# Kernel optimization log

Hardware: AMD Instinct MI355X
Metric: run time of the kernel (lower is better)

The kernel has to match this reference:

```python
import jax, jax.numpy as jnp
import numpy as np

BN_EPS = 1e-3


def _three_nn(unknown, known):
    # unknown: [B, N2, 3] query points; known: [B, N1, 3]
    # returns squared distances and indices of the 3 nearest known points
    # (CUDA three_nn returns squared euclidean distances).
    d2 = (jnp.sum(unknown * unknown, -1)[:, :, None]
          + jnp.sum(known * known, -1)[:, None, :]
          - 2.0 * jnp.einsum('bnd,bmd->bnm', unknown, known))  # [B, N2, N1]
    neg_top, ind = jax.lax.top_k(-d2, 3)                        # [B, N2, 3]
    dist2 = jnp.maximum(-neg_top, 0.0)
    return dist2, ind


def _conv_bn_relu(x, W, b, gamma, beta, mean, var):
    # x: [B, C_in, N]; W: [C_out, C_in] (1x1 conv); inference-mode BN
    y = jnp.einsum('oc,bcn->bon', W, x) + b[None, :, None]
    scale = gamma / jnp.sqrt(var + BN_EPS)
    y = (y - mean[None, :, None]) * scale[None, :, None] + beta[None, :, None]
    return jax.nn.relu(y)


def setup_inputs() -> dict:
    key = jax.random.key(0)
    ks = jax.random.split(key, 12)
    B, N1, N2, C1, C2, H = 2, 4096, 16384, 256, 128, 256
    return {
        'points1': jax.random.normal(ks[0], (B, 3, N1), jnp.float32),
        'points2': jax.random.normal(ks[1], (B, 3, N2), jnp.float32),
        'features1': jax.random.normal(ks[2], (B, C1, N1), jnp.float32),
        'features2': jax.random.normal(ks[3], (B, C2, N2), jnp.float32),
        'W1': jax.random.normal(ks[4], (H, C1 + C2), jnp.float32) * 0.05,
        'b1': jax.random.normal(ks[5], (H,), jnp.float32) * 0.05,
        'gamma1': jnp.ones((H,), jnp.float32),
        'beta1': jnp.zeros((H,), jnp.float32),
        'mean1': jax.random.normal(ks[6], (H,), jnp.float32) * 0.1,
        'var1': jax.random.uniform(ks[7], (H,), jnp.float32, 0.5, 1.5),
        'W2': jax.random.normal(ks[8], (H, H), jnp.float32) * 0.05,
        'b2': jax.random.normal(ks[9], (H,), jnp.float32) * 0.05,
        'gamma2': jnp.ones((H,), jnp.float32),
        'beta2': jnp.zeros((H,), jnp.float32),
        'mean2': jax.random.normal(ks[10], (H,), jnp.float32) * 0.1,
        'var2': jax.random.uniform(ks[11], (H,), jnp.float32, 0.5, 1.5),
    }


def reference(points1, points2, features1, features2,
              W1, b1, gamma1, beta1, mean1, var1,
              W2, b2, gamma2, beta2, mean2, var2):
    # 3-NN of each dense point (points2) among coarse points (points1)
    unknown = jnp.swapaxes(points2, 1, 2)  # [B, N2, 3]
    known = jnp.swapaxes(points1, 1, 2)    # [B, N1, 3]
    dist, ind = _three_nn(unknown, known)  # dist: squared distances [B, N2, 3]
    dist = dist * dist                     # forward squares again (as in source)
    dist = jnp.maximum(dist, 1e-10)
    inv = 1.0 / dist
    weights = inv / jnp.sum(inv, axis=2, keepdims=True)  # [B, N2, 3]

    # gather features of the 3 neighbors: features1 [B, C1, N1] -> [B, N2, 3, C1]
    f1 = jnp.swapaxes(features1, 1, 2)  # [B, N1, C1]
    gathered = jax.vmap(lambda f, i: f[i])(f1, ind)  # [B, N2, 3, C1]
    interp = jnp.einsum('bnkc,bnk->bcn', gathered, weights)  # [B, C1, N2]

    x = jnp.concatenate([interp, features2], axis=1)  # [B, C1+C2, N2]
    x = _conv_bn_relu(x, W1, b1, gamma1, beta1, mean1, var1)
    x = _conv_bn_relu(x, W2, b2, gamma2, beta2, mean2, var2)
    return x
```

## Files before the change

### kernel.cpp

```cpp
#include <hip/hip_runtime.h>
#include <cstdint>
#include <cstddef>

#define N1 4096
#define N2 16384
#define C1 256
#define C2 128
#define HH 256
#define K1 384
#define BQ 32768
#define KPAD 392
#define NCH 8

typedef float  f32x4  __attribute__((ext_vector_type(4)));
typedef __bf16 bf16x8 __attribute__((ext_vector_type(8)));
typedef __bf16 bf16x4 __attribute__((ext_vector_type(4)));

__device__ __forceinline__ float exact_dd(float ux, float uy, float uz,
                                          float su, float4 p) {
  float dot = __fadd_rn(__fadd_rn(__fmul_rn(ux, p.x), __fmul_rn(uy, p.y)),
                        __fmul_rn(uz, p.z));
  return __builtin_fmaf(dot, -2.0f, __fadd_rn(su, p.w));
}

__device__ __forceinline__ float4 load_pt(const float* __restrict__ p1b,
                                          int j) {
  float x = p1b[j], y = p1b[N1 + j], z = p1b[2 * N1 + j];
  float sk = __fadd_rn(__fadd_rn(__fmul_rn(x, x), __fmul_rn(y, y)),
                       __fmul_rn(z, z));
  return make_float4(x, y, z, sk);
}

#define LEXINS(da, db, dc, ia, ib, ic, dd, jj)                                 \
  {                                                                            \
    bool ca = ((dd) < (da)) || ((dd) == (da) && (jj) < (ia));                  \
    bool cb = ((dd) < (db)) || ((dd) == (db) && (jj) < (ib));                  \
    bool cc = ((dd) < (dc)) || ((dd) == (dc) && (jj) < (ic));                  \
    dc = cb ? (db) : (cc ? (dd) : (dc));                                       \
    ic = cb ? (ib) : (cc ? (jj) : (ic));                                       \
    db = ca ? (da) : (cb ? (dd) : (db));                                       \
    ib = ca ? (ia) : (cb ? (jj) : (ib));                                       \
    da = ca ? (dd) : (da);                                                     \
    ia = ca ? (jj) : (ia);                                                     \
  }

#define KMIN4(K1_, K2_, K3_, K4_, x)                                           \
  {                                                                            \
    float n1 = fminf((K1_), (x));                                              \
    float n2 = __builtin_amdgcn_fmed3f((K1_), (x), (K2_));                     \
    float n3 = __builtin_amdgcn_fmed3f((K2_), (x), (K3_));                     \
    float n4 = __builtin_amdgcn_fmed3f((K3_), (x), (K4_));                     \
    K1_ = n1; K2_ = n2; K3_ = n3; K4_ = n4;                                    \
  }

#define POINTQ(ux, uy, uz, su, px, py, pz, pw, jj, Ka, Kb, Kc, Kd)             \
  {                                                                            \
    float dot_ = __fadd_rn(                                                    \
        __fadd_rn(__fmul_rn((ux), (px)), __fmul_rn((uy), (py))),               \
        __fmul_rn((uz), (pz)));                                                \
    float dd_ = __builtin_fmaf(dot_, -2.0f, __fadd_rn((su), (pw)));            \
    float xk_ = __uint_as_float((__float_as_uint(dd_) & 0xFFFFF000u) |         \
                                ((unsigned)(jj) & 0x00000FFFu));               \
    KMIN4(Ka, Kb, Kc, Kd, xk_);                                                \
  }

__global__ __launch_bounds__(256) void k_front(
    const float* __restrict__ p1, const float* __restrict__ p2,
    const float* __restrict__ f1,
    const float* __restrict__ W1, const float* __restrict__ W2,
    const float* __restrict__ b1, const float* __restrict__ g1,
    const float* __restrict__ be1, const float* __restrict__ mm1,
    const float* __restrict__ vv1,
    const float* __restrict__ b2, const float* __restrict__ g2,
    const float* __restrict__ be2, const float* __restrict__ mm2,
    const float* __restrict__ vv2,
    __bf16* __restrict__ W1b, __bf16* __restrict__ W2b,
    float* __restrict__ scsh, float* __restrict__ f1T,
    float* __restrict__ keybuf) {
#pragma clang fp contract(off)
  __shared__ __align__(16) float smemf[64 * 65];
  const int bx = blockIdx.x;
  const int t = threadIdx.x;

  if (bx < 384) {
    int idx = bx * 256 + t;
    if (idx < HH * K1) W1b[idx] = (__bf16)W1[idx];
    if (idx < HH * HH) W2b[idx] = (__bf16)W2[idx];
    if (idx < HH) {
      float sc = g1[idx] / sqrtf(vv1[idx] + 1e-3f);
      scsh[idx]          = sc;
      scsh[HH + idx]     = fmaf(b1[idx] - mm1[idx], sc, be1[idx]);
      float s2 = g2[idx] / sqrtf(vv2[idx] + 1e-3f);
      scsh[2 * HH + idx] = s2;
      scsh[3 * HH + idx] = fmaf(b2[idx] - mm2[idx], s2, be2[idx]);
    }
    return;
  }

  if (bx < 896) {
    float (*tile)[65] = (float(*)[65])smemf;
    const int bz = bx - 384;
    const int b = bz >> 8;
    const int rest = bz & 255;
    const int ct = rest >> 6;
    const int ntb = (rest & 63) << 6;
    const int ln = t & 63, g = t >> 6;

    const float* src = f1 + ((size_t)b * C1 + ct * 64) * N1 + ntb;
    for (int k = 0; k < 16; ++k) {
      int c = (k << 2) + g;
      tile[c][ln] = src[(size_t)c * N1 + ln];
    }
    __syncthreads();
    float* dst = f1T + ((size_t)b * N1 + ntb) * C1 + ct * 64;
    for (int k = 0; k < 16; ++k) {
      int nn = (k << 2) + g;
      dst[(size_t)nn * C1 + ln] = tile[ln][nn];
    }
    return;
  }

  float4* spts = (float4*)smemf;
  const int bz = bx - 896;
  const int ch = bz & (NCH - 1);
  const int qt = bz >> 3;
  const int b  = qt >> 5;
  const int nA = ((qt & 31) << 9) + t;
  const int nB = nA + 256;

  const float* p1b = p1 + (size_t)b * 3 * N1;
  {
    int j = ch * 512 + t;
    spts[t]       = load_pt(p1b, j);
    spts[t + 256] = load_pt(p1b, j + 256);
  }

  const float* p2b = p2 + (size_t)b * 3 * N2;
  float uxA = p2b[nA], uyA = p2b[N2 + nA], uzA = p2b[2 * N2 + nA];
  float suA = __fadd_rn(__fadd_rn(__fmul_rn(uxA, uxA), __fmul_rn(uyA, uyA)),
                        __fmul_rn(uzA, uzA));
  float uxB = p2b[nB], uyB = p2b[N2 + nB], uzB = p2b[2 * N2 + nB];
  float suB = __fadd_rn(__fadd_rn(__fmul_rn(uxB, uxB), __fmul_rn(uyB, uyB)),
                        __fmul_rn(uzB, uzB));
  __syncthreads();

  const int j0 = ch * 512;
  float KaA = 3.0e38f, KbA = 3.0e38f, KcA = 3.0e38f, KdA = 3.0e38f;
  float KaB = 3.0e38f, KbB = 3.0e38f, KcB = 3.0e38f, KdB = 3.0e38f;
#pragma unroll 4
  for (int k = 0; k < 256; ++k) {
    float4 p0 = spts[2 * k];
    float4 p1v = spts[2 * k + 1];
    int i0 = j0 + 2 * k;
    int i1 = j0 + 2 * k + 1;
    POINTQ(uxA, uyA, uzA, suA, p0.x, p0.y, p0.z, p0.w, i0, KaA, KbA, KcA, KdA);
    POINTQ(uxA, uyA, uzA, suA, p1v.x, p1v.y, p1v.z, p1v.w, i1, KaA, KbA, KcA, KdA);
    POINTQ(uxB, uyB, uzB, suB, p0.x, p0.y, p0.z, p0.w, i0, KaB, KbB, KcB, KdB);
    POINTQ(uxB, uyB, uzB, suB, p1v.x, p1v.y, p1v.z, p1v.w, i1, KaB, KbB, KcB, KdB);
  }

  int qA = b * N2 + nA;
  int qB = b * N2 + nB;
  keybuf[(ch * 4 + 0) * BQ + qA] = KaA;
  keybuf[(ch * 4 + 1) * BQ + qA] = KbA;
  keybuf[(ch * 4 + 2) * BQ + qA] = KcA;
  keybuf[(ch * 4 + 3) * BQ + qA] = KdA;
  keybuf[(ch * 4 + 0) * BQ + qB] = KaB;
  keybuf[(ch * 4 + 1) * BQ + qB] = KbB;
  keybuf[(ch * 4 + 2) * BQ + qB] = KcB;
  keybuf[(ch * 4 + 3) * BQ + qB] = KdB;
}

__global__ __launch_bounds__(256) void k_merge(
    const float* __restrict__ keybuf, const float* __restrict__ p1,
    const float* __restrict__ p2,
    float* __restrict__ wbuf, int* __restrict__ ibuf) {
#pragma clang fp contract(off)
  int tid = blockIdx.x * 256 + threadIdx.x;
  int sub = tid & 3;
  int q = tid >> 2;
  int b = q >> 14, n = q & (N2 - 1);

  const float* p2b = p2 + (size_t)b * 3 * N2;
  float ux = p2b[n], uy = p2b[N2 + n], uz = p2b[2 * N2 + n];
  float su = __fadd_rn(__fadd_rn(__fmul_rn(ux, ux), __fmul_rn(uy, uy)),
                       __fmul_rn(uz, uz));

  float Ka = 3.0e38f, Kb = 3.0e38f, Kc = 3.0e38f, Kd = 3.0e38f;
#pragma unroll 4
  for (int m = 0; m < 8; ++m) {
    float x = keybuf[(sub * 8 + m) * BQ + q];
    KMIN4(Ka, Kb, Kc, Kd, x);
  }
#pragma unroll
  for (int msk = 1; msk <= 2; msk <<= 1) {
    float ea = __shfl_xor(Ka, msk, 64), eb = __shfl_xor(Kb, msk, 64);
    float ec = __shfl_xor(Kc, msk, 64), ed = __shfl_xor(Kd, msk, 64);
    KMIN4(Ka, Kb, Kc, Kd, ea);
    KMIN4(Ka, Kb, Kc, Kd, eb);
    KMIN4(Ka, Kb, Kc, Kd, ec);
    KMIN4(Ka, Kb, Kc, Kd, ed);
  }
  if (sub != 0) return;

  bool flag = (__float_as_uint(Kc) >> 12) == (__float_as_uint(Kd) >> 12);
  const float* p1b = p1 + (size_t)b * 3 * N1;
  float da, db, dc;
  int ia, ib, ic;
  if (!flag) {
    ia = (int)(__float_as_uint(Ka) & 0xFFFu);
    ib = (int)(__float_as_uint(Kb) & 0xFFFu);
    ic = (int)(__float_as_uint(Kc) & 0xFFFu);
    da = exact_dd(ux, uy, uz, su, load_pt(p1b, ia));
    db = exact_dd(ux, uy, uz, su, load_pt(p1b, ib));
    dc = exact_dd(ux, uy, uz, su, load_pt(p1b, ic));
  } else {
    da = 3.0e38f; db = 3.0e38f; dc = 3.0e38f;
    ia = 0x7fffffff; ib = 0x7fffffff; ic = 0x7fffffff;
    for (int i = 0; i < 4 * NCH; ++i) {
      float x = keybuf[i * BQ + q];
      int jj = (int)(__float_as_uint(x) & 0xFFFu);
      float dd = exact_dd(ux, uy, uz, su, load_pt(p1b, jj));
      LEXINS(da, db, dc, ia, ib, ic, dd, jj);
    }
  }

  float qa = fmaxf(da, 0.0f), qb = fmaxf(db, 0.0f), qc = fmaxf(dc, 0.0f);
  qa = fmaxf(__fmul_rn(qa, qa), 1e-10f);
  qb = fmaxf(__fmul_rn(qb, qb), 1e-10f);
  qc = fmaxf(__fmul_rn(qc, qc), 1e-10f);
  float va = __fdiv_rn(1.0f, qa);
  float vb = __fdiv_rn(1.0f, qb);
  float vc = __fdiv_rn(1.0f, qc);
  float s = __fadd_rn(__fadd_rn(va, vb), vc);
  wbuf[q]           = __fdiv_rn(va, s);
  wbuf[BQ + q]      = __fdiv_rn(vb, s);
  wbuf[2 * BQ + q]  = __fdiv_rn(vc, s);
  ibuf[q]          = ia;
  ibuf[BQ + q]     = ib;
  ibuf[2 * BQ + q] = ic;
}

__global__ __launch_bounds__(512) void k_fused(
    const float* __restrict__ f1T, const float* __restrict__ f2,
    const float* __restrict__ wbuf, const int* __restrict__ ibuf,
    const __bf16* __restrict__ W1b, const __bf16* __restrict__ W2b,
    const float* __restrict__ scsh, float* __restrict__ out) {
  __shared__ __bf16 sX[64 * KPAD];
  const int t = threadIdx.x;
  const int bx = blockIdx.x;
  const int b = bx >> 8;
  const int n0 = (bx & 255) << 6;

  {
    const int nn = t >> 3, qq = t & 7;
    const int gi = b * N2 + n0 + nn;
    const float w0 = wbuf[gi], w1 = wbuf[BQ + gi], w2 = wbuf[2 * BQ + gi];
    const int i0 = ibuf[gi], i1 = ibuf[BQ + gi], i2 = ibuf[2 * BQ + gi];
    const float4* r0 = (const float4*)(f1T + ((size_t)b * N1 + i0) * C1);
    const float4* r1 = (const float4*)(f1T + ((size_t)b * N1 + i1) * C1);
    const float4* r2 = (const float4*)(f1T + ((size_t)b * N1 + i2) * C1);
#pragma unroll 4
    for (int m = 0; m < 8; ++m) {
      int idx4 = (qq << 3) + m;
      float4 a = r0[idx4], c4 = r1[idx4], d4 = r2[idx4];
      bf16x4 v;
      v[0] = (__bf16)fmaf(w0, a.x, fmaf(w1, c4.x, w2 * d4.x));
      v[1] = (__bf16)fmaf(w0, a.y, fmaf(w1, c4.y, w2 * d4.y));
      v[2] = (__bf16)fmaf(w0, a.z, fmaf(w1, c4.z, w2 * d4.z));
      v[3] = (__bf16)fmaf(w0, a.w, fmaf(w1, c4.w, w2 * d4.w));
      *(bf16x4*)&sX[nn * KPAD + (idx4 << 2)] = v;
    }
  }
  {
    const int col = t & 63, g = t >> 6;
    const float* f2b = f2 + (size_t)b * C2 * N2 + n0 + col;
#pragma unroll
    for (int m = 0; m < 4; ++m) {
      int c4 = (g << 4) + (m << 2);
      bf16x4 v;
      v[0] = (__bf16)f2b[(size_t)(c4 + 0) * N2];
      v[1] = (__bf16)f2b[(size_t)(c4 + 1) * N2];
      v[2] = (__bf16)f2b[(size_t)(c4 + 2) * N2];
      v[3] = (__bf16)f2b[(size_t)(c4 + 3) * N2];
      *(bf16x4*)&sX[col * KPAD + 256 + c4] = v;
    }
  }
  __syncthreads();

  const int l  = t & 63;
  const int wv = __builtin_amdgcn_readfirstlane(t >> 6);
  const int ob = wv << 5;
  const int lm = l & 15, lg = l >> 4;

  f32x4 acc[2][4];
#pragma unroll
  for (int mt = 0; mt < 2; ++mt)
#pragma unroll
    for (int nt = 0; nt < 4; ++nt) acc[mt][nt] = (f32x4)0.0f;

  for (int ks = 0; ks < 12; ++ks) {
    bf16x8 af[2], bfr[4];
#pragma unroll
    for (int mt = 0; mt < 2; ++mt)
      af[mt] = *(const bf16x8*)(W1b + (size_t)(ob + mt * 16 + lm) * K1 +
                                ks * 32 + lg * 8);
#pragma unroll
    for (int nt = 0; nt < 4; ++nt)
      bfr[nt] = *(const bf16x8*)&sX[(nt * 16 + lm) * KPAD + ks * 32 + lg * 8];
#pragma unroll
    for (int mt = 0; mt < 2; ++mt)
#pragma unroll
      for (int nt = 0; nt < 4; ++nt)
        acc[mt][nt] = __builtin_amdgcn_mfma_f32_16x16x32_bf16(
            af[mt], bfr[nt], acc[mt][nt], 0, 0, 0);
  }
  __syncthreads();

#pragma unroll
  for (int mt = 0; mt < 2; ++mt) {
    int rb = ob + mt * 16 + lg * 4;
    float4 sc4 = *(const float4*)(scsh + rb);
    float4 sh4 = *(const float4*)(scsh + HH + rb);
#pragma unroll
    for (int nt = 0; nt < 4; ++nt) {
      int colc = nt * 16 + lm;
      bf16x4 v;
      v[0] = (__bf16)fmaxf(fmaf(acc[mt][nt][0], sc4.x, sh4.x), 0.0f);
      v[1] = (__bf16)fmaxf(fmaf(acc[mt][nt][1], sc4.y, sh4.y), 0.0f);
      v[2] = (__bf16)fmaxf(fmaf(acc[mt][nt][2], sc4.z, sh4.z), 0.0f);
      v[3] = (__bf16)fmaxf(fmaf(acc[mt][nt][3], sc4.w, sh4.w), 0.0f);
      *(bf16x4*)&sX[colc * KPAD + rb] = v;
    }
  }
  __syncthreads();

  f32x4 ac2[2][4];
#pragma unroll
  for (int mt = 0; mt < 2; ++mt)
#pragma unroll
    for (int nt = 0; nt < 4; ++nt) ac2[mt][nt] = (f32x4)0.0f;
  for (int ks = 0; ks < 8; ++ks) {
    bf16x8 af[2], bfr[4];
#pragma unroll
    for (int mt = 0; mt < 2; ++mt)
      af[mt] = *(const bf16x8*)(W2b + (size_t)(ob + mt * 16 + lm) * HH +
                                ks * 32 + lg * 8);
#pragma unroll
    for (int nt = 0; nt < 4; ++nt)
      bfr[nt] = *(const bf16x8*)&sX[(nt * 16 + lm) * KPAD + ks * 32 + lg * 8];
#pragma unroll
    for (int mt = 0; mt < 2; ++mt)
#pragma unroll
      for (int nt = 0; nt < 4; ++nt)
        ac2[mt][nt] = __builtin_amdgcn_mfma_f32_16x16x32_bf16(
            af[mt], bfr[nt], ac2[mt][nt], 0, 0, 0);
  }

  float* outb = out + (size_t)b * HH * N2 + n0;
#pragma unroll
  for (int mt = 0; mt < 2; ++mt) {
    int rb = ob + mt * 16 + lg * 4;
    float4 sc4 = *(const float4*)(scsh + 2 * HH + rb);
    float4 sh4 = *(const float4*)(scsh + 3 * HH + rb);
#pragma unroll
    for (int nt = 0; nt < 4; ++nt) {
      int colc = nt * 16 + lm;
      outb[(size_t)(rb + 0) * N2 + colc] =
          fmaxf(fmaf(ac2[mt][nt][0], sc4.x, sh4.x), 0.0f);
      outb[(size_t)(rb + 1) * N2 + colc] =
          fmaxf(fmaf(ac2[mt][nt][1], sc4.y, sh4.y), 0.0f);
      outb[(size_t)(rb + 2) * N2 + colc] =
          fmaxf(fmaf(ac2[mt][nt][2], sc4.z, sh4.z), 0.0f);
      outb[(size_t)(rb + 3) * N2 + colc] =
          fmaxf(fmaf(ac2[mt][nt][3], sc4.w, sh4.w), 0.0f);
    }
  }
}

extern "C" void kernel_launch(void* const* d_in, const int* in_sizes, int n_in,
                              void* d_out, int out_size, void* d_ws, size_t ws_size,
                              hipStream_t stream) {
  const float* p1  = (const float*)d_in[0];
  const float* p2  = (const float*)d_in[1];
  const float* f1  = (const float*)d_in[2];
  const float* f2  = (const float*)d_in[3];
  const float* W1  = (const float*)d_in[4];
  const float* bb1 = (const float*)d_in[5];
  const float* g1  = (const float*)d_in[6];
  const float* be1 = (const float*)d_in[7];
  const float* mm1 = (const float*)d_in[8];
  const float* vv1 = (const float*)d_in[9];
  const float* W2  = (const float*)d_in[10];
  const float* bb2 = (const float*)d_in[11];
  const float* g2  = (const float*)d_in[12];
  const float* be2 = (const float*)d_in[13];
  const float* mm2 = (const float*)d_in[14];
  const float* vv2 = (const float*)d_in[15];
  float* out = (float*)d_out;

  char* ws = (char*)d_ws;
  float*  f1T    = (float*)(ws);
  float*  keybuf = (float*)(ws + 8388608);
  float*  wbuf   = (float*)(ws + 12582912);
  int*    ibuf   = (int*)  (ws + 12976128);
  __bf16* W1b    = (__bf16*)(ws + 13369344);
  __bf16* W2b    = (__bf16*)(ws + 13565952);
  float*  scsh   = (float*)(ws + 13697024);

  k_front<<<1408, 256, 0, stream>>>(p1, p2, f1, W1, W2,
                                    bb1, g1, be1, mm1, vv1,
                                    bb2, g2, be2, mm2, vv2,
                                    W1b, W2b, scsh, f1T, keybuf);
  k_merge<<<512, 256, 0, stream>>>(keybuf, p1, p2, wbuf, ibuf);
  k_fused<<<512, 512, 0, stream>>>(f1T, f2, wbuf, ibuf, W1b, W2b, scsh, out);
}
```

Before: 106.4 us.

## Fuse top-3 merge and weight computation into the fused gather/MLP kernel

Removes the separate k_merge kernel and does the 32-candidate key merge, exact distance recompute and inverse-distance weights inside k_fused, with 8 threads per point reducing via shuffles. This drops one launch and the write/read of wbuf/ibuf. The tie fallback now brute-forces all 4096 points split across 8 lanes rather than rechecking only the 32 candidates. Launch bounds also request 2 blocks per CU, which may constrain registers.

```diff
diff --git a/kernel.cpp b/kernel.cpp
--- a/kernel.cpp
+++ b/kernel.cpp
@@ -171,79 +171,10 @@
   keybuf[(ch * 4 + 3) * BQ + qB] = KdB;
 }
 
-__global__ __launch_bounds__(256) void k_merge(
-    const float* __restrict__ keybuf, const float* __restrict__ p1,
-    const float* __restrict__ p2,
-    float* __restrict__ wbuf, int* __restrict__ ibuf) {
-#pragma clang fp contract(off)
-  int tid = blockIdx.x * 256 + threadIdx.x;
-  int sub = tid & 3;
-  int q = tid >> 2;
-  int b = q >> 14, n = q & (N2 - 1);
-
-  const float* p2b = p2 + (size_t)b * 3 * N2;
-  float ux = p2b[n], uy = p2b[N2 + n], uz = p2b[2 * N2 + n];
-  float su = __fadd_rn(__fadd_rn(__fmul_rn(ux, ux), __fmul_rn(uy, uy)),
-                       __fmul_rn(uz, uz));
-
-  float Ka = 3.0e38f, Kb = 3.0e38f, Kc = 3.0e38f, Kd = 3.0e38f;
-#pragma unroll 4
-  for (int m = 0; m < 8; ++m) {
-    float x = keybuf[(sub * 8 + m) * BQ + q];
-    KMIN4(Ka, Kb, Kc, Kd, x);
-  }
-#pragma unroll
-  for (int msk = 1; msk <= 2; msk <<= 1) {
-    float ea = __shfl_xor(Ka, msk, 64), eb = __shfl_xor(Kb, msk, 64);
-    float ec = __shfl_xor(Kc, msk, 64), ed = __shfl_xor(Kd, msk, 64);
-    KMIN4(Ka, Kb, Kc, Kd, ea);
-    KMIN4(Ka, Kb, Kc, Kd, eb);
-    KMIN4(Ka, Kb, Kc, Kd, ec);
-    KMIN4(Ka, Kb, Kc, Kd, ed);
-  }
-  if (sub != 0) return;
-
-  bool flag = (__float_as_uint(Kc) >> 12) == (__float_as_uint(Kd) >> 12);
-  const float* p1b = p1 + (size_t)b * 3 * N1;
-  float da, db, dc;
-  int ia, ib, ic;
-  if (!flag) {
-    ia = (int)(__float_as_uint(Ka) & 0xFFFu);
-    ib = (int)(__float_as_uint(Kb) & 0xFFFu);
-    ic = (int)(__float_as_uint(Kc) & 0xFFFu);
-    da = exact_dd(ux, uy, uz, su, load_pt(p1b, ia));
-    db = exact_dd(ux, uy, uz, su, load_pt(p1b, ib));
-    dc = exact_dd(ux, uy, uz, su, load_pt(p1b, ic));
-  } else {
-    da = 3.0e38f; db = 3.0e38f; dc = 3.0e38f;
-    ia = 0x7fffffff; ib = 0x7fffffff; ic = 0x7fffffff;
-    for (int i = 0; i < 4 * NCH; ++i) {
-      float x = keybuf[i * BQ + q];
-      int jj = (int)(__float_as_uint(x) & 0xFFFu);
-      float dd = exact_dd(ux, uy, uz, su, load_pt(p1b, jj));
-      LEXINS(da, db, dc, ia, ib, ic, dd, jj);
-    }
-  }
-
-  float qa = fmaxf(da, 0.0f), qb = fmaxf(db, 0.0f), qc = fmaxf(dc, 0.0f);
-  qa = fmaxf(__fmul_rn(qa, qa), 1e-10f);
-  qb = fmaxf(__fmul_rn(qb, qb), 1e-10f);
-  qc = fmaxf(__fmul_rn(qc, qc), 1e-10f);
-  float va = __fdiv_rn(1.0f, qa);
-  float vb = __fdiv_rn(1.0f, qb);
-  float vc = __fdiv_rn(1.0f, qc);
-  float s = __fadd_rn(__fadd_rn(va, vb), vc);
-  wbuf[q]           = __fdiv_rn(va, s);
-  wbuf[BQ + q]      = __fdiv_rn(vb, s);
-  wbuf[2 * BQ + q]  = __fdiv_rn(vc, s);
-  ibuf[q]          = ia;
-  ibuf[BQ + q]     = ib;
-  ibuf[2 * BQ + q] = ic;
-}
-
-__global__ __launch_bounds__(512) void k_fused(
+__global__ __launch_bounds__(512, 2) void k_fused(
     const float* __restrict__ f1T, const float* __restrict__ f2,
-    const float* __restrict__ wbuf, const int* __restrict__ ibuf,
+    const float* __restrict__ p2, const float* __restrict__ p1,
+    const float* __restrict__ keybuf,
     const __bf16* __restrict__ W1b, const __bf16* __restrict__ W2b,
     const float* __restrict__ scsh, float* __restrict__ out) {
   __shared__ __bf16 sX[64 * KPAD];
@@ -252,11 +183,81 @@
   const int b = bx >> 8;
   const int n0 = (bx & 255) << 6;
 
+  float w0, w1, w2;
+  int i0, i1, i2;
   {
-    const int nn = t >> 3, qq = t & 7;
-    const int gi = b * N2 + n0 + nn;
-    const float w0 = wbuf[gi], w1 = wbuf[BQ + gi], w2 = wbuf[2 * BQ + gi];
-    const int i0 = ibuf[gi], i1 = ibuf[BQ + gi], i2 = ibuf[2 * BQ + gi];
+#pragma clang fp contract(off)
+    const int sub = t & 7, col = t >> 3;
+    const int n = n0 + col;
+    const int gi = b * N2 + n;
+    const float* p2b = p2 + (size_t)b * 3 * N2;
+    float ux = p2b[n], uy = p2b[N2 + n], uz = p2b[2 * N2 + n];
+    float su = __fadd_rn(__fadd_rn(__fmul_rn(ux, ux), __fmul_rn(uy, uy)),
+                         __fmul_rn(uz, uz));
+
+    float Ka = 3.0e38f, Kb = 3.0e38f, Kc = 3.0e38f, Kd = 3.0e38f;
+#pragma unroll
+    for (int m = 0; m < 4; ++m) {
+      float x = keybuf[(sub * 4 + m) * BQ + gi];
+      KMIN4(Ka, Kb, Kc, Kd, x);
+    }
+#pragma unroll
+    for (int msk = 1; msk <= 4; msk <<= 1) {
+      float ea = __shfl_xor(Ka, msk, 64), eb = __shfl_xor(Kb, msk, 64);
+      float ec = __shfl_xor(Kc, msk, 64), ed = __shfl_xor(Kd, msk, 64);
+      KMIN4(Ka, Kb, Kc, Kd, ea);
+      KMIN4(Ka, Kb, Kc, Kd, eb);
+      KMIN4(Ka, Kb, Kc, Kd, ec);
+      KMIN4(Ka, Kb, Kc, Kd, ed);
+    }
+    bool flag = (__float_as_uint(Kc) >> 12) == (__float_as_uint(Kd) >> 12);
+
+    const float* p1b = p1 + (size_t)b * 3 * N1;
+    float da, db, dc;
+    int ia, ib, ic;
+    if (!flag) {
+      ia = (int)(__float_as_uint(Ka) & 0xFFFu);
+      ib = (int)(__float_as_uint(Kb) & 0xFFFu);
+      ic = (int)(__float_as_uint(Kc) & 0xFFFu);
+      da = exact_dd(ux, uy, uz, su, load_pt(p1b, ia));
+      db = exact_dd(ux, uy, uz, su, load_pt(p1b, ib));
+      dc = exact_dd(ux, uy, uz, su, load_pt(p1b, ic));
+    } else {
+      da = 3.0e38f; db = 3.0e38f; dc = 3.0e38f;
+      ia = 0x7fffffff; ib = 0x7fffffff; ic = 0x7fffffff;
+      for (int k = 0; k < 512; ++k) {
+        int j = (k << 3) + sub;
+        float dd = exact_dd(ux, uy, uz, su, load_pt(p1b, j));
+        LEXINS(da, db, dc, ia, ib, ic, dd, j);
+      }
+#pragma unroll
+      for (int msk = 1; msk <= 4; msk <<= 1) {
+        float ea = __shfl_xor(da, msk, 64), eb = __shfl_xor(db, msk, 64),
+              ec = __shfl_xor(dc, msk, 64);
+        int ja = __shfl_xor(ia, msk, 64), jb = __shfl_xor(ib, msk, 64),
+            jc = __shfl_xor(ic, msk, 64);
+        LEXINS(da, db, dc, ia, ib, ic, ea, ja);
+        LEXINS(da, db, dc, ia, ib, ic, eb, jb);
+        LEXINS(da, db, dc, ia, ib, ic, ec, jc);
+      }
+    }
+
+    float qa = fmaxf(da, 0.0f), qb = fmaxf(db, 0.0f), qc = fmaxf(dc, 0.0f);
+    qa = fmaxf(__fmul_rn(qa, qa), 1e-10f);
+    qb = fmaxf(__fmul_rn(qb, qb), 1e-10f);
+    qc = fmaxf(__fmul_rn(qc, qc), 1e-10f);
+    float va = __fdiv_rn(1.0f, qa);
+    float vb = __fdiv_rn(1.0f, qb);
+    float vc = __fdiv_rn(1.0f, qc);
+    float s = __fadd_rn(__fadd_rn(va, vb), vc);
+    w0 = __fdiv_rn(va, s);
+    w1 = __fdiv_rn(vb, s);
+    w2 = __fdiv_rn(vc, s);
+    i0 = ia; i1 = ib; i2 = ic;
+  }
+
+  {
+    const int qq = t & 7;
     const float4* r0 = (const float4*)(f1T + ((size_t)b * N1 + i0) * C1);
     const float4* r1 = (const float4*)(f1T + ((size_t)b * N1 + i1) * C1);
     const float4* r2 = (const float4*)(f1T + ((size_t)b * N1 + i2) * C1);
@@ -269,7 +270,7 @@
       v[1] = (__bf16)fmaf(w0, a.y, fmaf(w1, c4.y, w2 * d4.y));
       v[2] = (__bf16)fmaf(w0, a.z, fmaf(w1, c4.z, w2 * d4.z));
       v[3] = (__bf16)fmaf(w0, a.w, fmaf(w1, c4.w, w2 * d4.w));
-      *(bf16x4*)&sX[nn * KPAD + (idx4 << 2)] = v;
+      *(bf16x4*)&sX[(t >> 3) * KPAD + (idx4 << 2)] = v;
     }
   }
   {
@@ -402,16 +403,14 @@
   char* ws = (char*)d_ws;
   float*  f1T    = (float*)(ws);
   float*  keybuf = (float*)(ws + 8388608);
-  float*  wbuf   = (float*)(ws + 12582912);
-  int*    ibuf   = (int*)  (ws + 12976128);
-  __bf16* W1b    = (__bf16*)(ws + 13369344);
-  __bf16* W2b    = (__bf16*)(ws + 13565952);
-  float*  scsh   = (float*)(ws + 13697024);
+  __bf16* W1b    = (__bf16*)(ws + 12582912);
+  __bf16* W2b    = (__bf16*)(ws + 12779520);
+  float*  scsh   = (float*)(ws + 12910592);
 
   k_front<<<1408, 256, 0, stream>>>(p1, p2, f1, W1, W2,
                                     bb1, g1, be1, mm1, vv1,
                                     bb2, g2, be2, mm2, vv2,
                                     W1b, W2b, scsh, f1T, keybuf);
-  k_merge<<<512, 256, 0, stream>>>(keybuf, p1, p2, wbuf, ibuf);
-  k_fused<<<512, 512, 0, stream>>>(f1T, f2, wbuf, ibuf, W1b, W2b, scsh, out);
+  k_fused<<<512, 512, 0, stream>>>(f1T, f2, p2, p1, keybuf,
+                                   W1b, W2b, scsh, out);
 }
```

Result: slower. 225.8 us (+112.2%).
